# Performance work log

Hardware: AMD Instinct MI355X
Metric: run time of the kernel (lower is better)

Reference implementation:

```python
import jax, jax.numpy as jnp
import numpy as np

GROUPS = 32
HEADS = 4
EPS_GN = 1e-5
EPS_DEN = 1e-6


def group_norm(x, gamma, beta):
    b, c, h, w = x.shape
    xg = x.reshape(b, GROUPS, (c // GROUPS) * h * w)
    mu = xg.mean(axis=-1, keepdims=True)
    var = xg.var(axis=-1, keepdims=True)
    xn = ((xg - mu) * jax.lax.rsqrt(var + EPS_GN)).reshape(b, c, h, w)
    return xn * gamma[None, :, None, None] + beta[None, :, None, None]


def setup_inputs() -> dict:
    key = jax.random.key(0)
    ks = jax.random.split(key, 4)
    b, c, h, w = 16, 256, 64, 64
    x = jax.random.normal(ks[0], (b, c, h, w), dtype=jnp.float32)
    gamma = jnp.ones((c,), jnp.float32)
    beta = jnp.zeros((c,), jnp.float32)
    w_qkv = jax.random.normal(ks[1], (3 * c, c), jnp.float32) * (1.0 / np.sqrt(c))
    b_qkv = jnp.zeros((3 * c,), jnp.float32)
    w_out = jax.random.normal(ks[2], (c, c), jnp.float32) * (1.0 / np.sqrt(c))
    b_out = jnp.zeros((c,), jnp.float32)
    return {"x": x, "gamma": gamma, "beta": beta, "w_qkv": w_qkv,
            "b_qkv": b_qkv, "w_out": w_out, "b_out": b_out}


def reference(x, gamma, beta, w_qkv, b_qkv, w_out, b_out):
    b, c, h, w = x.shape
    d = c // HEADS
    n = h * w
    xn = group_norm(x, gamma, beta)
    # 1x1 conv == channel GEMM: [b,3c,h,w]
    qkv = jnp.einsum('bchw,oc->bohw', xn, w_qkv) + b_qkv[None, :, None, None]
    q, k, v = jnp.split(qkv, 3, axis=1)
    # b (heads d) h w -> b heads d n
    q = q.reshape(b, HEADS, d, n)
    k = k.reshape(b, HEADS, d, n)
    v = v.reshape(b, HEADS, d, n)
    q = jax.nn.elu(q) + 1.0
    k = jax.nn.elu(k) + 1.0
    k_sum = k.sum(axis=-1)                                 # [b,H,d]
    kv = jnp.einsum('bhdn,bhen->bhde', k, v)               # [b,H,d,d]
    out = jnp.einsum('bhde,bhdn->bhen', kv, q)             # [b,H,d,n]
    denom = jnp.einsum('bhdn,bhd->bhn', q, k_sum)          # [b,H,n]
    out = out / (denom[:, :, None, :] + EPS_DEN)
    out = out.reshape(b, c, h, w)
    out = jnp.einsum('bchw,oc->bohw', out, w_out) + b_out[None, :, None, None]
    return out + x
```

## Files before the change

### kernel.cpp

```cpp
#include <hip/hip_runtime.h>
#include <stdint.h>

#define BATCH 16
#define CH    256
#define NSP   4096
#define NH    4
#define HD    64

typedef __attribute__((ext_vector_type(8))) short bf16x8;
typedef __attribute__((ext_vector_type(4))) float f32x4;
typedef __attribute__((ext_vector_type(4))) unsigned int u32x4;

__device__ __forceinline__ short f2bf(float f) {
    union { float f; unsigned u; } v; v.f = f;
    unsigned r = (v.u + 0x7fffu + ((v.u >> 16) & 1u)) >> 16;
    return (short)r;
}
__device__ __forceinline__ float bf2f(short s) {
    union { float f; unsigned u; } v; v.u = ((unsigned)(unsigned short)s) << 16;
    return v.f;
}

__global__ __launch_bounds__(256) void k_pre(
        const float* __restrict__ x, const float* __restrict__ wq, const float* __restrict__ wo,
        float* __restrict__ mu, float* __restrict__ rstd,
        short* __restrict__ wq_bf, short* __restrict__ wo_bf) {
    int bg = blockIdx.x;
    if (bg < 512) {
        const float4* p = (const float4*)(x + (size_t)bg * 32768);
        float s = 0.f, sq = 0.f;
        for (int i = threadIdx.x; i < 8192; i += 256) {
            float4 v = p[i];
            s  += v.x + v.y + v.z + v.w;
            sq += v.x * v.x + v.y * v.y + v.z * v.z + v.w * v.w;
        }
        for (int off = 32; off; off >>= 1) { s += __shfl_down(s, off); sq += __shfl_down(sq, off); }
        __shared__ float ls[4], lq[4];
        int w = threadIdx.x >> 6;
        if ((threadIdx.x & 63) == 0) { ls[w] = s; lq[w] = sq; }
        __syncthreads();
        if (threadIdx.x == 0) {
            float S = ls[0] + ls[1] + ls[2] + ls[3];
            float Q = lq[0] + lq[1] + lq[2] + lq[3];
            float m = S / 32768.f;
            float var = Q / 32768.f - m * m;
            mu[bg] = m; rstd[bg] = rsqrtf(var + 1e-5f);
        }
    } else {
        int idx = ((bg - 512) * 256 + threadIdx.x) * 4;
        float4 v;
        short* dst;
        if (idx < 196608) { v = *(const float4*)(wq + idx); dst = wq_bf + idx; }
        else              { v = *(const float4*)(wo + (idx - 196608)); dst = wo_bf + (idx - 196608); }
        unsigned p0 = ((unsigned)(unsigned short)f2bf(v.x)) | (((unsigned)(unsigned short)f2bf(v.y)) << 16);
        unsigned p1 = ((unsigned)(unsigned short)f2bf(v.z)) | (((unsigned)(unsigned short)f2bf(v.w)) << 16);
        uint2 pk; pk.x = p0; pk.y = p1;
        *(uint2*)dst = pk;
    }
}

__global__ __launch_bounds__(256) void k_gnqkv(
        const float* __restrict__ x, const float* __restrict__ gamma, const float* __restrict__ beta,
        const float* __restrict__ mu, const float* __restrict__ rstd,
        const short* __restrict__ wq_bf, const float* __restrict__ b_qkv,
        short* __restrict__ q_t, float* __restrict__ kvp, float* __restrict__ ksp) {
    int b = blockIdx.y, nt = blockIdx.x;
    int n0 = nt * 64;
    __shared__ short Blds[64 * 264];
    __shared__ short Asm[128 * 40];
    __shared__ union UR {
        struct { short kst[64 * 72]; short vst[64 * 72]; } s;
        short cst[64 * 136];
    } R;
    int t = threadIdx.x, lane = t & 63, wv = t >> 6, lr = lane & 15, quad = lane >> 4;

    {
        const float* xb = x + (size_t)b * CH * NSP;
        int m = t & 15, cq = t >> 4;
        for (int cb = 0; cb < 16; cb++) {
            int c = cb * 16 + cq;
            int g = c >> 3;
            float sc = rstd[b * 32 + g] * gamma[c];
            float sh = beta[c] - mu[b * 32 + g] * sc;
            float4 v = *(const float4*)(xb + (size_t)c * NSP + n0 + m * 4);
            float vv[4] = {v.x, v.y, v.z, v.w};
            #pragma unroll
            for (int j = 0; j < 4; j++) {
                int n = m * 4 + j;
                int cc = c ^ (((n >> 4) & 3) << 3);
                Blds[n * 264 + cc] = f2bf(vv[j] * sc + sh);
            }
        }
    }
    __syncthreads();

    for (int h = 0; h < 4; h++) {
        for (int pass = 0; pass < 2; pass++) {
            int base = (pass ? 512 : 256) + h * 64;
            f32x4 acc[2][2] = {};
            int wm = (wv & 1) * 32, wn = (wv >> 1) * 32;
            for (int k0 = 0; k0 < 256; k0 += 32) {
                int row = t >> 2, kc = (t & 3) * 8;
                *(u32x4*)(Asm + row * 40 + kc) = *(const u32x4*)(wq_bf + (size_t)(base + row) * 256 + k0 + kc);
                __syncthreads();
                bf16x8 afr[2], bfr[2];
                #pragma unroll
                for (int mi = 0; mi < 2; mi++) afr[mi] = *(const bf16x8*)(Asm + (wm + mi * 16 + lr) * 40 + quad * 8);
                #pragma unroll
                for (int ni = 0; ni < 2; ni++) {
                    int rr = wn + ni * 16 + lr;
                    bfr[ni] = *(const bf16x8*)(Blds + rr * 264 + ((k0 + quad * 8) ^ (((rr >> 4) & 3) << 3)));
                }
                #pragma unroll
                for (int mi = 0; mi < 2; mi++)
                    #pragma unroll
                    for (int ni = 0; ni < 2; ni++)
                        acc[mi][ni] = __builtin_amdgcn_mfma_f32_16x16x32_bf16(afr[mi], bfr[ni], acc[mi][ni], 0, 0, 0);
                __syncthreads();
            }
            short* dst = pass ? R.s.vst : R.s.kst;
            #pragma unroll
            for (int mi = 0; mi < 2; mi++)
              #pragma unroll
              for (int ni = 0; ni < 2; ni++)
                #pragma unroll
                for (int r = 0; r < 4; r++) {
                    int ol = wm + mi * 16 + quad * 4 + r;
                    int nl = wn + ni * 16 + lr;
                    float v = acc[mi][ni][r] + b_qkv[base + ol];
                    if (!pass) v = v > 0.f ? v + 1.f : __expf(v);
                    dst[ol * 72 + nl] = f2bf(v);
                }
            __syncthreads();
            if (!pass) {
                int d = t >> 2, nq = (t & 3) * 16;
                float s = 0.f;
                #pragma unroll
                for (int j = 0; j < 16; j++) s += bf2f(R.s.kst[d * 72 + nq + j]);
                s += __shfl_down(s, 2);
                s += __shfl_down(s, 1);
                if ((t & 3) == 0) ksp[((size_t)(b * 4 + h) * 64 + nt) * 64 + d] = s;
            }
        }
        f32x4 acc2[4] = {};
        #pragma unroll
        for (int kk = 0; kk < 64; kk += 32) {
            bf16x8 af = *(const bf16x8*)(R.s.vst + (wv * 16 + lr) * 72 + kk + quad * 8);
            bf16x8 bfk[4];
            #pragma unroll
            for (int ni = 0; ni < 4; ni++)
                bfk[ni] = *(const bf16x8*)(R.s.kst + (ni * 16 + lr) * 72 + kk + quad * 8);
            #pragma unroll
            for (int ni = 0; ni < 4; ni++)
                acc2[ni] = __builtin_amdgcn_mfma_f32_16x16x32_bf16(af, bfk[ni], acc2[ni], 0, 0, 0);
        }
        float* kvdst = kvp + ((size_t)(b * 4 + h) * 64 + nt) * 4096;
        #pragma unroll
        for (int ni = 0; ni < 4; ni++)
            #pragma unroll
            for (int r = 0; r < 4; r++)
                kvdst[(wv * 16 + quad * 4 + r) * 64 + ni * 16 + lr] = acc2[ni][r];
    }

    for (int mtq = 0; mtq < 2; mtq++) {
        f32x4 acc[4][2] = {};
        int wm = (wv & 1) * 64, wn = (wv >> 1) * 32;
        for (int k0 = 0; k0 < 256; k0 += 32) {
            #pragma unroll
            for (int i = 0; i < 2; i++) {
                int ch = t + i * 256;
                int row = ch >> 2, kc = (ch & 3) * 8;
                *(u32x4*)(Asm + row * 40 + kc) = *(const u32x4*)(wq_bf + (size_t)(mtq * 128 + row) * 256 + k0 + kc);
            }
            __syncthreads();
            bf16x8 afr[4], bfr[2];
            #pragma unroll
            for (int mi = 0; mi < 4; mi++) afr[mi] = *(const bf16x8*)(Asm + (wm + mi * 16 + lr) * 40 + quad * 8);
            #pragma unroll
            for (int ni = 0; ni < 2; ni++) {
                int rr = wn + ni * 16 + lr;
                bfr[ni] = *(const bf16x8*)(Blds + rr * 264 + ((k0 + quad * 8) ^ (((rr >> 4) & 3) << 3)));
            }
            #pragma unroll
            for (int mi = 0; mi < 4; mi++)
                #pragma unroll
                for (int ni = 0; ni < 2; ni++)
                    acc[mi][ni] = __builtin_amdgcn_mfma_f32_16x16x32_bf16(afr[mi], bfr[ni], acc[mi][ni], 0, 0, 0);
            __syncthreads();
        }
        #pragma unroll
        for (int mi = 0; mi < 4; mi++)
          #pragma unroll
          for (int ni = 0; ni < 2; ni++)
            #pragma unroll
            for (int r = 0; r < 4; r++) {
                int ol = wm + mi * 16 + quad * 4 + r;
                int nl = wn + ni * 16 + lr;
                float v = acc[mi][ni][r] + b_qkv[mtq * 128 + ol];
                v = v > 0.f ? v + 1.f : __expf(v);
                R.cst[nl * 136 + ol] = f2bf(v);
            }
        __syncthreads();
        #pragma unroll
        for (int i = 0; i < 4; i++) {
            int ch = t + i * 256;
            int row = ch >> 4, o8 = (ch & 15) * 8;
            int hh = mtq * 2 + (o8 >> 6), d0 = o8 & 63;
            *(u32x4*)(q_t + ((size_t)(b * 4 + hh) * NSP + n0 + row) * HD + d0) =
                *(const u32x4*)(R.cst + row * 136 + o8);
        }
        __syncthreads();
    }
}

__global__ __launch_bounds__(256) void k_kv_reduce(
        const float* __restrict__ kvp, const float* __restrict__ ksp,
        float* __restrict__ kvT_g, float* __restrict__ ksum_g) {
    int eq = blockIdx.x, bh = blockIdx.y;
    int t = threadIdx.x;
    const float* base = kvp + (size_t)bh * 64 * 4096 + eq * 1024;
    float4 s = {0.f, 0.f, 0.f, 0.f};
    for (int ntc = 0; ntc < 64; ntc++) {
        float4 v = *(const float4*)(base + (size_t)ntc * 4096 + t * 4);
        s.x += v.x; s.y += v.y; s.z += v.z; s.w += v.w;
    }
    *(float4*)(kvT_g + (size_t)bh * 4096 + eq * 1024 + t * 4) = s;
    if (eq == 0 && t < 64) {
        float ss = 0.f;
        for (int ntc = 0; ntc < 64; ntc++) ss += ksp[((size_t)bh * 64 + ntc) * 64 + t];
        ksum_g[bh * 64 + t] = ss;
    }
}

__global__ __launch_bounds__(256) void k_attn_out(
        const short* __restrict__ q_t, const float* __restrict__ kvT_g,
        const float* __restrict__ ksum_g, const short* __restrict__ wo_bf,
        const float* __restrict__ b_out, const float* __restrict__ x,
        float* __restrict__ out) {
    int b = blockIdx.y, nt = blockIdx.x;
    int n0 = nt * 64;
    __shared__ short Battn[64 * 264];
    __shared__ union UR {
        struct { short ql[64 * 72]; short kvl[64 * 72]; } a;
        short Asm2[128 * 40];
    } R;
    __shared__ float ksl[64], dnl[64];
    int t = threadIdx.x, lane = t & 63, wv = t >> 6, lr = lane & 15, quad = lane >> 4;

    for (int h = 0; h < 4; h++) {
        int bh = b * 4 + h;
        #pragma unroll
        for (int i = 0; i < 2; i++) {
            int ch = t + i * 256;
            int row = ch >> 3, dc = (ch & 7) * 8;
            *(u32x4*)(R.a.ql + row * 72 + dc) =
                *(const u32x4*)(q_t + ((size_t)bh * NSP + n0 + row) * HD + dc);
        }
        const float* kvg = kvT_g + (size_t)bh * 4096;
        for (int i = t; i < 4096; i += 256)
            R.a.kvl[(i >> 6) * 72 + (i & 63)] = f2bf(kvg[i]);
        if (t < 64) ksl[t] = ksum_g[bh * 64 + t];
        __syncthreads();
        if (t < 64) {
            float s = 0.f;
            #pragma unroll
            for (int d = 0; d < 64; d++) s += bf2f(R.a.ql[t * 72 + d]) * ksl[d];
            dnl[t] = 1.f / (s + 1e-6f);
        }
        __syncthreads();
        f32x4 acc[4] = {};
        #pragma unroll
        for (int kk = 0; kk < 64; kk += 32) {
            bf16x8 af = *(const bf16x8*)(R.a.ql + (wv * 16 + lr) * 72 + kk + quad * 8);
            bf16x8 bfr[4];
            #pragma unroll
            for (int ni = 0; ni < 4; ni++)
                bfr[ni] = *(const bf16x8*)(R.a.kvl + (ni * 16 + lr) * 72 + kk + quad * 8);
            #pragma unroll
            for (int ni = 0; ni < 4; ni++)
                acc[ni] = __builtin_amdgcn_mfma_f32_16x16x32_bf16(af, bfr[ni], acc[ni], 0, 0, 0);
        }
        float dn[4];
        #pragma unroll
        for (int r = 0; r < 4; r++) dn[r] = dnl[wv * 16 + quad * 4 + r];
        #pragma unroll
        for (int ni = 0; ni < 4; ni++)
            #pragma unroll
            for (int r = 0; r < 4; r++) {
                int n = wv * 16 + quad * 4 + r;
                int e = ni * 16 + lr;
                Battn[n * 264 + h * 64 + e] = f2bf(acc[ni][r] * dn[r]);
            }
        __syncthreads();
    }

    for (int p = 0; p < 2; p++) {
        f32x4 acc[4][2] = {};
        int wm = (wv & 1) * 64, wn = (wv >> 1) * 32;
        for (int k0 = 0; k0 < 256; k0 += 32) {
            #pragma unroll
            for (int i = 0; i < 2; i++) {
                int ch = t + i * 256;
                int row = ch >> 2, kc = (ch & 3) * 8;
                *(u32x4*)(R.Asm2 + row * 40 + kc) =
                    *(const u32x4*)(wo_bf + (size_t)(p * 128 + row) * 256 + k0 + kc);
            }
            __syncthreads();
            bf16x8 afr[4], bfr[2];
            #pragma unroll
            for (int mi = 0; mi < 4; mi++) afr[mi] = *(const bf16x8*)(R.Asm2 + (wm + mi * 16 + lr) * 40 + quad * 8);
            #pragma unroll
            for (int ni = 0; ni < 2; ni++)
                bfr[ni] = *(const bf16x8*)(Battn + (wn + ni * 16 + lr) * 264 + k0 + quad * 8);
            #pragma unroll
            for (int mi = 0; mi < 4; mi++)
                #pragma unroll
                for (int ni = 0; ni < 2; ni++)
                    acc[mi][ni] = __builtin_amdgcn_mfma_f32_16x16x32_bf16(afr[mi], bfr[ni], acc[mi][ni], 0, 0, 0);
            __syncthreads();
        }
        #pragma unroll
        for (int mi = 0; mi < 4; mi++)
          #pragma unroll
          for (int ni = 0; ni < 2; ni++)
            #pragma unroll
            for (int r = 0; r < 4; r++) {
                int ol = wm + mi * 16 + quad * 4 + r;
                int nl = wn + ni * 16 + lr;
                int o = p * 128 + ol;
                size_t idx = ((size_t)b * CH + o) * NSP + n0 + nl;
                out[idx] = acc[mi][ni][r] + b_out[o] + x[idx];
            }
    }
}

extern "C" void kernel_launch(void* const* d_in, const int* in_sizes, int n_in,
                              void* d_out, int out_size, void* d_ws, size_t ws_size,
                              hipStream_t stream) {
    const float* x     = (const float*)d_in[0];
    const float* gamma = (const float*)d_in[1];
    const float* beta  = (const float*)d_in[2];
    const float* w_qkv = (const float*)d_in[3];
    const float* b_qkv = (const float*)d_in[4];
    const float* w_out = (const float*)d_in[5];
    const float* b_out = (const float*)d_in[6];
    float* out = (float*)d_out;

    char* ws = (char*)d_ws;
    size_t off = 0;
    float* mu    = (float*)(ws + off); off += 2048;
    float* rstd  = (float*)(ws + off); off += 2048;
    short* wq_bf = (short*)(ws + off); off += (size_t)768 * 256 * 2;
    short* wo_bf = (short*)(ws + off); off += (size_t)256 * 256 * 2;
    short* q_t   = (short*)(ws + off); off += (size_t)BATCH * NSP * CH * 2;
    float* kvp   = (float*)(ws + off); off += (size_t)64 * 64 * 4096 * 4;
    float* ksp   = (float*)(ws + off); off += (size_t)64 * 64 * 64 * 4;
    float* kvT_g = (float*)(ws + off); off += (size_t)64 * 4096 * 4;
    float* ksum_g = (float*)(ws + off); off += (size_t)64 * 64 * 4;

    if (ws_size < off) return;

    k_pre<<<768, 256, 0, stream>>>(x, w_qkv, w_out, mu, rstd, wq_bf, wo_bf);
    k_gnqkv<<<dim3(64, 16), 256, 0, stream>>>(x, gamma, beta, mu, rstd, wq_bf, b_qkv, q_t, kvp, ksp);
    k_kv_reduce<<<dim3(4, 64), 256, 0, stream>>>(kvp, ksp, kvT_g, ksum_g);
    k_attn_out<<<dim3(64, 16), 256, 0, stream>>>(q_t, kvT_g, ksum_g, wo_bf, b_out, x, out);
}
```

Before: 283.2 us.

## Read weight fragments directly from global and store KV partials in bf16

The weight GEMM tiles now load MFMA A-fragments straight from global memory (relying on L2) instead of staging them through LDS with a barrier every k-step. Warps are retiled so each computes 32 rows by 64 columns, and the K and V projections are computed concurrently by different warps rather than in two sequential passes. The per-tile KV partials and the reduced KV matrix are stored in bf16 instead of fp32, halving that intermediate traffic, and the reduce kernel and attention load are adjusted to match. This trades LDS staging and barriers for uncoalesced global fragment loads, and adds bf16 rounding of the partial sums, which may reduce accuracy.

Result: faster. 259.7 us (-8.3%).

```diff
diff --git a/kernel.cpp b/kernel.cpp
--- a/kernel.cpp
+++ b/kernel.cpp
@@ -63,11 +63,10 @@
         const float* __restrict__ x, const float* __restrict__ gamma, const float* __restrict__ beta,
         const float* __restrict__ mu, const float* __restrict__ rstd,
         const short* __restrict__ wq_bf, const float* __restrict__ b_qkv,
-        short* __restrict__ q_t, float* __restrict__ kvp, float* __restrict__ ksp) {
+        short* __restrict__ q_t, short* __restrict__ kvp_bf, float* __restrict__ ksp) {
     int b = blockIdx.y, nt = blockIdx.x;
     int n0 = nt * 64;
     __shared__ short Blds[64 * 264];
-    __shared__ short Asm[128 * 40];
     __shared__ union UR {
         struct { short kst[64 * 72]; short vst[64 * 72]; } s;
         short cst[64 * 136];
@@ -95,52 +94,49 @@
     __syncthreads();
 
     for (int h = 0; h < 4; h++) {
-        for (int pass = 0; pass < 2; pass++) {
-            int base = (pass ? 512 : 256) + h * 64;
-            f32x4 acc[2][2] = {};
-            int wm = (wv & 1) * 32, wn = (wv >> 1) * 32;
-            for (int k0 = 0; k0 < 256; k0 += 32) {
-                int row = t >> 2, kc = (t & 3) * 8;
-                *(u32x4*)(Asm + row * 40 + kc) = *(const u32x4*)(wq_bf + (size_t)(base + row) * 256 + k0 + kc);
-                __syncthreads();
-                bf16x8 afr[2], bfr[2];
+        int base_row = (wv < 2 ? 256 : 512) + h * 64;
+        int sub = (wv & 1) * 32;
+        f32x4 acc[2][4] = {};
+        for (int k0 = 0; k0 < 256; k0 += 32) {
+            bf16x8 afr[2], bfr[4];
+            #pragma unroll
+            for (int mi = 0; mi < 2; mi++)
+                afr[mi] = *(const bf16x8*)(wq_bf + (size_t)(base_row + sub + mi * 16 + lr) * 256 + k0 + quad * 8);
+            #pragma unroll
+            for (int ni = 0; ni < 4; ni++) {
+                int rr = ni * 16 + lr;
+                bfr[ni] = *(const bf16x8*)(Blds + rr * 264 + ((k0 + quad * 8) ^ (((rr >> 4) & 3) << 3)));
+            }
+            #pragma unroll
+            for (int mi = 0; mi < 2; mi++)
                 #pragma unroll
-                for (int mi = 0; mi < 2; mi++) afr[mi] = *(const bf16x8*)(Asm + (wm + mi * 16 + lr) * 40 + quad * 8);
-                #pragma unroll
-                for (int ni = 0; ni < 2; ni++) {
-                    int rr = wn + ni * 16 + lr;
-                    bfr[ni] = *(const bf16x8*)(Blds + rr * 264 + ((k0 + quad * 8) ^ (((rr >> 4) & 3) << 3)));
-                }
-                #pragma unroll
-                for (int mi = 0; mi < 2; mi++)
-                    #pragma unroll
-                    for (int ni = 0; ni < 2; ni++)
-                        acc[mi][ni] = __builtin_amdgcn_mfma_f32_16x16x32_bf16(afr[mi], bfr[ni], acc[mi][ni], 0, 0, 0);
-                __syncthreads();
-            }
-            short* dst = pass ? R.s.vst : R.s.kst;
-            #pragma unroll
-            for (int mi = 0; mi < 2; mi++)
-              #pragma unroll
-              for (int ni = 0; ni < 2; ni++)
-                #pragma unroll
-                for (int r = 0; r < 4; r++) {
-                    int ol = wm + mi * 16 + quad * 4 + r;
-                    int nl = wn + ni * 16 + lr;
-                    float v = acc[mi][ni][r] + b_qkv[base + ol];
-                    if (!pass) v = v > 0.f ? v + 1.f : __expf(v);
-                    dst[ol * 72 + nl] = f2bf(v);
-                }
-            __syncthreads();
-            if (!pass) {
-                int d = t >> 2, nq = (t & 3) * 16;
-                float s = 0.f;
-                #pragma unroll
-                for (int j = 0; j < 16; j++) s += bf2f(R.s.kst[d * 72 + nq + j]);
-                s += __shfl_down(s, 2);
-                s += __shfl_down(s, 1);
-                if ((t & 3) == 0) ksp[((size_t)(b * 4 + h) * 64 + nt) * 64 + d] = s;
-            }
+                for (int ni = 0; ni < 4; ni++)
+                    acc[mi][ni] = __builtin_amdgcn_mfma_f32_16x16x32_bf16(afr[mi], bfr[ni], acc[mi][ni], 0, 0, 0);
+        }
+        __syncthreads();
+        short* dst = (wv < 2) ? R.s.kst : R.s.vst;
+        bool is_k = (wv < 2);
+        #pragma unroll
+        for (int mi = 0; mi < 2; mi++)
+          #pragma unroll
+          for (int ni = 0; ni < 4; ni++)
+            #pragma unroll
+            for (int r = 0; r < 4; r++) {
+                int ol = sub + mi * 16 + quad * 4 + r;
+                int nl = ni * 16 + lr;
+                float v = acc[mi][ni][r] + b_qkv[base_row + ol];
+                if (is_k) v = v > 0.f ? v + 1.f : __expf(v);
+                dst[ol * 72 + nl] = f2bf(v);
+            }
+        __syncthreads();
+        {
+            int d = t >> 2, nq = (t & 3) * 16;
+            float s = 0.f;
+            #pragma unroll
+            for (int j = 0; j < 16; j++) s += bf2f(R.s.kst[d * 72 + nq + j]);
+            s += __shfl_down(s, 2);
+            s += __shfl_down(s, 1);
+            if ((t & 3) == 0) ksp[((size_t)(b * 4 + h) * 64 + nt) * 64 + d] = s;
         }
         f32x4 acc2[4] = {};
         #pragma unroll
@@ -154,48 +150,42 @@
             for (int ni = 0; ni < 4; ni++)
                 acc2[ni] = __builtin_amdgcn_mfma_f32_16x16x32_bf16(af, bfk[ni], acc2[ni], 0, 0, 0);
         }
-        float* kvdst = kvp + ((size_t)(b * 4 + h) * 64 + nt) * 4096;
+        short* kvdst = kvp_bf + ((size_t)(b * 4 + h) * 64 + nt) * 4096;
         #pragma unroll
         for (int ni = 0; ni < 4; ni++)
             #pragma unroll
             for (int r = 0; r < 4; r++)
-                kvdst[(wv * 16 + quad * 4 + r) * 64 + ni * 16 + lr] = acc2[ni][r];
+                kvdst[(wv * 16 + quad * 4 + r) * 64 + ni * 16 + lr] = f2bf(acc2[ni][r]);
     }
 
     for (int mtq = 0; mtq < 2; mtq++) {
-        f32x4 acc[4][2] = {};
-        int wm = (wv & 1) * 64, wn = (wv >> 1) * 32;
+        f32x4 acc[2][4] = {};
+        int wm = wv * 32;
         for (int k0 = 0; k0 < 256; k0 += 32) {
-            #pragma unroll
-            for (int i = 0; i < 2; i++) {
-                int ch = t + i * 256;
-                int row = ch >> 2, kc = (ch & 3) * 8;
-                *(u32x4*)(Asm + row * 40 + kc) = *(const u32x4*)(wq_bf + (size_t)(mtq * 128 + row) * 256 + k0 + kc);
-            }
-            __syncthreads();
-            bf16x8 afr[4], bfr[2];
-            #pragma unroll
-            for (int mi = 0; mi < 4; mi++) afr[mi] = *(const bf16x8*)(Asm + (wm + mi * 16 + lr) * 40 + quad * 8);
-            #pragma unroll
-            for (int ni = 0; ni < 2; ni++) {
-                int rr = wn + ni * 16 + lr;
+            bf16x8 afr[2], bfr[4];
+            #pragma unroll
+            for (int mi = 0; mi < 2; mi++)
+                afr[mi] = *(const bf16x8*)(wq_bf + (size_t)(mtq * 128 + wm + mi * 16 + lr) * 256 + k0 + quad * 8);
+            #pragma unroll
+            for (int ni = 0; ni < 4; ni++) {
+                int rr = ni * 16 + lr;
                 bfr[ni] = *(const bf16x8*)(Blds + rr * 264 + ((k0 + quad * 8) ^ (((rr >> 4) & 3) << 3)));
             }
             #pragma unroll
-            for (int mi = 0; mi < 4; mi++)
+            for (int mi = 0; mi < 2; mi++)
                 #pragma unroll
-                for (int ni = 0; ni < 2; ni++)
+                for (int ni = 0; ni < 4; ni++)
                     acc[mi][ni] = __builtin_amdgcn_mfma_f32_16x16x32_bf16(afr[mi], bfr[ni], acc[mi][ni], 0, 0, 0);
-            __syncthreads();
-        }
-        #pragma unroll
-        for (int mi = 0; mi < 4; mi++)
+        }
+        __syncthreads();
+        #pragma unroll
+        for (int mi = 0; mi < 2; mi++)
           #pragma unroll
-          for (int ni = 0; ni < 2; ni++)
+          for (int ni = 0; ni < 4; ni++)
             #pragma unroll
             for (int r = 0; r < 4; r++) {
                 int ol = wm + mi * 16 + quad * 4 + r;
-                int nl = wn + ni * 16 + lr;
+                int nl = ni * 16 + lr;
                 float v = acc[mi][ni][r] + b_qkv[mtq * 128 + ol];
                 v = v > 0.f ? v + 1.f : __expf(v);
                 R.cst[nl * 136 + ol] = f2bf(v);
@@ -209,23 +199,27 @@
             *(u32x4*)(q_t + ((size_t)(b * 4 + hh) * NSP + n0 + row) * HD + d0) =
                 *(const u32x4*)(R.cst + row * 136 + o8);
         }
-        __syncthreads();
     }
 }
 
 __global__ __launch_bounds__(256) void k_kv_reduce(
-        const float* __restrict__ kvp, const float* __restrict__ ksp,
-        float* __restrict__ kvT_g, float* __restrict__ ksum_g) {
-    int eq = blockIdx.x, bh = blockIdx.y;
+        const short* __restrict__ kvp_bf, const float* __restrict__ ksp,
+        short* __restrict__ kvT_bf, float* __restrict__ ksum_g) {
+    int p = blockIdx.x, bh = blockIdx.y;
     int t = threadIdx.x;
-    const float* base = kvp + (size_t)bh * 64 * 4096 + eq * 1024;
-    float4 s = {0.f, 0.f, 0.f, 0.f};
+    int chunk = p * 256 + t;
+    const short* base = kvp_bf + (size_t)bh * 64 * 4096 + chunk * 8;
+    float s[8] = {};
     for (int ntc = 0; ntc < 64; ntc++) {
-        float4 v = *(const float4*)(base + (size_t)ntc * 4096 + t * 4);
-        s.x += v.x; s.y += v.y; s.z += v.z; s.w += v.w;
-    }
-    *(float4*)(kvT_g + (size_t)bh * 4096 + eq * 1024 + t * 4) = s;
-    if (eq == 0 && t < 64) {
+        bf16x8 v = *(const bf16x8*)(base + (size_t)ntc * 4096);
+        #pragma unroll
+        for (int j = 0; j < 8; j++) s[j] += bf2f(v[j]);
+    }
+    bf16x8 rv;
+    #pragma unroll
+    for (int j = 0; j < 8; j++) rv[j] = f2bf(s[j]);
+    *(bf16x8*)(kvT_bf + (size_t)bh * 4096 + chunk * 8) = rv;
+    if (p == 0 && t < 64) {
         float ss = 0.f;
         for (int ntc = 0; ntc < 64; ntc++) ss += ksp[((size_t)bh * 64 + ntc) * 64 + t];
         ksum_g[bh * 64 + t] = ss;
@@ -233,17 +227,15 @@
 }
 
 __global__ __launch_bounds__(256) void k_attn_out(
-        const short* __restrict__ q_t, const float* __restrict__ kvT_g,
+        const short* __restrict__ q_t, const short* __restrict__ kvT_bf,
         const float* __restrict__ ksum_g, const short* __restrict__ wo_bf,
         const float* __restrict__ b_out, const float* __restrict__ x,
         float* __restrict__ out) {
     int b = blockIdx.y, nt = blockIdx.x;
     int n0 = nt * 64;
     __shared__ short Battn[64 * 264];
-    __shared__ union UR {
-        struct { short ql[64 * 72]; short kvl[64 * 72]; } a;
-        short Asm2[128 * 40];
-    } R;
+    __shared__ short ql[64 * 72];
+    __shared__ short kvl[64 * 72];
     __shared__ float ksl[64], dnl[64];
     int t = threadIdx.x, lane = t & 63, wv = t >> 6, lr = lane & 15, quad = lane >> 4;
 
@@ -253,29 +245,28 @@
         for (int i = 0; i < 2; i++) {
             int ch = t + i * 256;
             int row = ch >> 3, dc = (ch & 7) * 8;
-            *(u32x4*)(R.a.ql + row * 72 + dc) =
+            *(u32x4*)(ql + row * 72 + dc) =
                 *(const u32x4*)(q_t + ((size_t)bh * NSP + n0 + row) * HD + dc);
-        }
-        const float* kvg = kvT_g + (size_t)bh * 4096;
-        for (int i = t; i < 4096; i += 256)
-            R.a.kvl[(i >> 6) * 72 + (i & 63)] = f2bf(kvg[i]);
+            *(u32x4*)(kvl + row * 72 + dc) =
+                *(const u32x4*)(kvT_bf + (size_t)bh * 4096 + row * 64 + dc);
+        }
         if (t < 64) ksl[t] = ksum_g[bh * 64 + t];
         __syncthreads();
         if (t < 64) {
             float s = 0.f;
             #pragma unroll
-            for (int d = 0; d < 64; d++) s += bf2f(R.a.ql[t * 72 + d]) * ksl[d];
+            for (int d = 0; d < 64; d++) s += bf2f(ql[t * 72 + d]) * ksl[d];
             dnl[t] = 1.f / (s + 1e-6f);
         }
         __syncthreads();
         f32x4 acc[4] = {};
         #pragma unroll
         for (int kk = 0; kk < 64; kk += 32) {
-            bf16x8 af = *(const bf16x8*)(R.a.ql + (wv * 16 + lr) * 72 + kk + quad * 8);
+            bf16x8 af = *(const bf16x8*)(ql + (wv * 16 + lr) * 72 + kk + quad * 8);
             bf16x8 bfr[4];
             #pragma unroll
             for (int ni = 0; ni < 4; ni++)
-                bfr[ni] = *(const bf16x8*)(R.a.kvl + (ni * 16 + lr) * 72 + kk + quad * 8);
+                bfr[ni] = *(const bf16x8*)(kvl + (ni * 16 + lr) * 72 + kk + quad * 8);
             #pragma unroll
             for (int ni = 0; ni < 4; ni++)
                 acc[ni] = __builtin_amdgcn_mfma_f32_16x16x32_bf16(af, bfr[ni], acc[ni], 0, 0, 0);
@@ -288,46 +279,36 @@
             #pragma unroll
             for (int r = 0; r < 4; r++) {
                 int n = wv * 16 + quad * 4 + r;
-                int e = ni * 16 + lr;
-                Battn[n * 264 + h * 64 + e] = f2bf(acc[ni][r] * dn[r]);
+                Battn[n * 264 + h * 64 + ni * 16 + lr] = f2bf(acc[ni][r] * dn[r]);
             }
         __syncthreads();
     }
 
     for (int p = 0; p < 2; p++) {
-        f32x4 acc[4][2] = {};
-        int wm = (wv & 1) * 64, wn = (wv >> 1) * 32;
+        f32x4 acc[2][4] = {};
+        int wm = wv * 32;
         for (int k0 = 0; k0 < 256; k0 += 32) {
-            #pragma unroll
-            for (int i = 0; i < 2; i++) {
-                int ch = t + i * 256;
-                int row = ch >> 2, kc = (ch & 3) * 8;
-                *(u32x4*)(R.Asm2 + row * 40 + kc) =
-                    *(const u32x4*)(wo_bf + (size_t)(p * 128 + row) * 256 + k0 + kc);
-            }
-            __syncthreads();
-            bf16x8 afr[4], bfr[2];
-            #pragma unroll
-            for (int mi = 0; mi < 4; mi++) afr[mi] = *(const bf16x8*)(R.Asm2 + (wm + mi * 16 + lr) * 40 + quad * 8);
-            #pragma unroll
-            for (int ni = 0; ni < 2; ni++)
-                bfr[ni] = *(const bf16x8*)(Battn + (wn + ni * 16 + lr) * 264 + k0 + quad * 8);
-            #pragma unroll
-            for (int mi = 0; mi < 4; mi++)
+            bf16x8 afr[2], bfr[4];
+            #pragma unroll
+            for (int mi = 0; mi < 2; mi++)
+                afr[mi] = *(const bf16x8*)(wo_bf + (size_t)(p * 128 + wm + mi * 16 + lr) * 256 + k0 + quad * 8);
+            #pragma unroll
+            for (int ni = 0; ni < 4; ni++)
+                bfr[ni] = *(const bf16x8*)(Battn + (ni * 16 + lr) * 264 + k0 + quad * 8);
+            #pragma unroll
+            for (int mi = 0; mi < 2; mi++)
                 #pragma unroll
-                for (int ni = 0; ni < 2; ni++)
+                for (int ni = 0; ni < 4; ni++)
                     acc[mi][ni] = __builtin_amdgcn_mfma_f32_16x16x32_bf16(afr[mi], bfr[ni], acc[mi][ni], 0, 0, 0);
-            __syncthreads();
-        }
-        #pragma unroll
-        for (int mi = 0; mi < 4; mi++)
+        }
+        #pragma unroll
+        for (int mi = 0; mi < 2; mi++)
           #pragma unroll
-          for (int ni = 0; ni < 2; ni++)
+          for (int ni = 0; ni < 4; ni++)
             #pragma unroll
             for (int r = 0; r < 4; r++) {
-                int ol = wm + mi * 16 + quad * 4 + r;
-                int nl = wn + ni * 16 + lr;
-                int o = p * 128 + ol;
+                int o = p * 128 + wm + mi * 16 + quad * 4 + r;
+                int nl = ni * 16 + lr;
                 size_t idx = ((size_t)b * CH + o) * NSP + n0 + nl;
                 out[idx] = acc[mi][ni][r] + b_out[o] + x[idx];
             }
@@ -348,20 +329,20 @@
 
     char* ws = (char*)d_ws;
     size_t off = 0;
-    float* mu    = (float*)(ws + off); off += 2048;
-    float* rstd  = (float*)(ws + off); off += 2048;
-    short* wq_bf = (short*)(ws + off); off += (size_t)768 * 256 * 2;
-    short* wo_bf = (short*)(ws + off); off += (size_t)256 * 256 * 2;
-    short* q_t   = (short*)(ws + off); off += (size_t)BATCH * NSP * CH * 2;
-    float* kvp   = (float*)(ws + off); off += (size_t)64 * 64 * 4096 * 4;
-    float* ksp   = (float*)(ws + off); off += (size_t)64 * 64 * 64 * 4;
-    float* kvT_g = (float*)(ws + off); off += (size_t)64 * 4096 * 4;
+    float* mu     = (float*)(ws + off); off += 2048;
+    float* rstd   = (float*)(ws + off); off += 2048;
+    short* wq_bf  = (short*)(ws + off); off += (size_t)768 * 256 * 2;
+    short* wo_bf  = (short*)(ws + off); off += (size_t)256 * 256 * 2;
+    short* q_t    = (short*)(ws + off); off += (size_t)BATCH * NSP * CH * 2;
+    short* kvp_bf = (short*)(ws + off); off += (size_t)64 * 64 * 4096 * 2;
+    float* ksp    = (float*)(ws + off); off += (size_t)64 * 64 * 64 * 4;
+    short* kvT_bf = (short*)(ws + off); off += (size_t)64 * 4096 * 2;
     float* ksum_g = (float*)(ws + off); off += (size_t)64 * 64 * 4;
 
     if (ws_size < off) return;
 
     k_pre<<<768, 256, 0, stream>>>(x, w_qkv, w_out, mu, rstd, wq_bf, wo_bf);
-    k_gnqkv<<<dim3(64, 16), 256, 0, stream>>>(x, gamma, beta, mu, rstd, wq_bf, b_qkv, q_t, kvp, ksp);
-    k_kv_reduce<<<dim3(4, 64), 256, 0, stream>>>(kvp, ksp, kvT_g, ksum_g);
-    k_attn_out<<<dim3(64, 16), 256, 0, stream>>>(q_t, kvT_g, ksum_g, wo_bf, b_out, x, out);
-}
+    k_gnqkv<<<dim3(64, 16), 256, 0, stream>>>(x, gamma, beta, mu, rstd, wq_bf, b_qkv, q_t, kvp_bf, ksp);
+    k_kv_reduce<<<dim3(2, 64), 256, 0, stream>>>(kvp_bf, ksp, kvT_bf, ksum_g);
+    k_attn_out<<<dim3(64, 16), 256, 0, stream>>>(q_t, kvT_bf, ksum_g, wo_bf, b_out, x, out);
+}
```
